# Kernel optimization log

Hardware: AMD Instinct MI355X
Metric: run time of the kernel (lower is better)

## Reference

```python
import jax, jax.numpy as jnp
import numpy as np

DIM = 512
NUM_HEADS = 8
HEAD_DIM = DIM // NUM_HEADS          # 64
KEY_DIM = int(HEAD_DIM * 0.5)        # 32
H_QKV = DIM + NUM_HEADS * KEY_DIM * 2  # 1024
SCALE = KEY_DIM ** -0.5
EPS = 1e-5


def bn(x, gamma, beta, mean, var):
    # inference-mode BatchNorm2d over channel axis 1 of NCHW
    inv = gamma / jnp.sqrt(var + EPS)
    return x * inv[None, :, None, None] + (beta - mean * inv)[None, :, None, None]


def conv1x1(x, w):
    # w: [out, in] (1x1 conv collapsed); x: NCHW
    return jnp.einsum('bchw,oc->bohw', x, w)


def dwconv3x3(x, w):
    # depthwise 3x3, 'same' padding; w: [C,1,3,3]
    return jax.lax.conv_general_dilated(
        x, w, window_strides=(1, 1), padding='SAME',
        feature_group_count=x.shape[1],
        dimension_numbers=('NCHW', 'OIHW', 'NCHW'))


def setup_inputs() -> dict:
    key = jax.random.key(0)
    ks = jax.random.split(key, 16)
    B, C, H, W = 8, DIM, 40, 40
    f = jax.random.normal
    inp = {
        'x': f(ks[0], (B, C, H, W), jnp.float32),
        'qkv_w': f(ks[1], (H_QKV, DIM), jnp.float32) * (1.0 / np.sqrt(DIM)),
        'qkv_gamma': 1.0 + 0.1 * f(ks[2], (H_QKV,), jnp.float32),
        'qkv_beta': 0.1 * f(ks[3], (H_QKV,), jnp.float32),
        'qkv_mean': 0.1 * f(ks[4], (H_QKV,), jnp.float32),
        'qkv_var': jax.random.uniform(ks[5], (H_QKV,), jnp.float32) + 0.5,
        'pe_w': f(ks[6], (DIM, 1, 3, 3), jnp.float32) * (1.0 / 3.0),
        'pe_gamma': 1.0 + 0.1 * f(ks[7], (DIM,), jnp.float32),
        'pe_beta': 0.1 * f(ks[8], (DIM,), jnp.float32),
        'pe_mean': 0.1 * f(ks[9], (DIM,), jnp.float32),
        'pe_var': jax.random.uniform(ks[10], (DIM,), jnp.float32) + 0.5,
        'proj_w': f(ks[11], (DIM, DIM), jnp.float32) * (1.0 / np.sqrt(DIM)),
        'proj_gamma': 1.0 + 0.1 * f(ks[12], (DIM,), jnp.float32),
        'proj_beta': 0.1 * f(ks[13], (DIM,), jnp.float32),
        'proj_mean': 0.1 * f(ks[14], (DIM,), jnp.float32),
        'proj_var': jax.random.uniform(ks[15], (DIM,), jnp.float32) + 0.5,
    }
    return inp


def reference(x, qkv_w, qkv_gamma, qkv_beta, qkv_mean, qkv_var,
              pe_w, pe_gamma, pe_beta, pe_mean, pe_var,
              proj_w, proj_gamma, proj_beta, proj_mean, proj_var):
    B, C, H, W = x.shape
    N = H * W
    qkv = bn(conv1x1(x, qkv_w), qkv_gamma, qkv_beta, qkv_mean, qkv_var)
    qkv = qkv.reshape(B, NUM_HEADS, KEY_DIM * 2 + HEAD_DIM, N)
    q = qkv[:, :, :KEY_DIM]                    # [B,h,kd,N]
    k = qkv[:, :, KEY_DIM:2 * KEY_DIM]         # [B,h,kd,N]
    v = qkv[:, :, 2 * KEY_DIM:]                # [B,h,hd,N]
    # attn = q^T @ k * scale -> [B,h,N,N], softmax over last dim
    attn = jnp.einsum('bhkn,bhkm->bhnm', q, k) * SCALE
    attn = jax.nn.softmax(attn, axis=-1)
    # out = v @ attn^T -> [B,h,hd,N]
    out = jnp.einsum('bhdm,bhnm->bhdn', v, attn).reshape(B, C, H, W)
    pe = bn(dwconv3x3(v.reshape(B, C, H, W), pe_w), pe_gamma, pe_beta, pe_mean, pe_var)
    y = out + pe
    y = bn(conv1x1(y, proj_w), proj_gamma, proj_beta, proj_mean, proj_var)
    return y
```

## Files before the change

### kernel.cpp

```cpp
#include <hip/hip_runtime.h>
#include <hip/hip_bf16.h>

#define EPS 1e-5f
#define SCALE 0.17677669529663687f
#define QSCALE 0.25500526817095634f

typedef __attribute__((ext_vector_type(8))) short bf16x8;
typedef __attribute__((ext_vector_type(4))) float f32x4;
typedef __attribute__((ext_vector_type(8))) unsigned short u16x8;

__device__ __forceinline__ unsigned short f2bf(float x) {
  union { float f; unsigned int u; } a; a.f = x;
  unsigned int r = a.u + 0x7FFFu + ((a.u >> 16) & 1u);
  return (unsigned short)(r >> 16);
}
__device__ __forceinline__ float bf2f(unsigned short u) {
  union { unsigned int u; float f; } a; a.u = ((unsigned int)u) << 16;
  return a.f;
}

__device__ __forceinline__ float fexp2(float x) {
#if __has_builtin(__builtin_amdgcn_exp2f)
  return __builtin_amdgcn_exp2f(x);
#else
  float r; asm("v_exp_f32 %0, %1" : "=v"(r) : "v"(x)); return r;
#endif
}

__device__ __forceinline__ void gload_lds16(const void* g, void* l) {
  __builtin_amdgcn_global_load_lds(
      (const __attribute__((address_space(1))) unsigned int*)g,
      (__attribute__((address_space(3))) unsigned int*)l, 16, 0, 0);
}

__device__ __forceinline__ unsigned int pack_bf_trunc(float a, float b) {
  return __builtin_amdgcn_perm(__float_as_uint(b), __float_as_uint(a), 0x07060302u);
}

__global__ __launch_bounds__(256) void cast_w_kernel(
    const float* __restrict__ qw, const float* __restrict__ pw,
    short* __restrict__ wq, short* __restrict__ wp) {
  int idx = blockIdx.x * 256 + threadIdx.x;
  const float4* src;
  ushort4* dst;
  if (idx < 131072) {
    src = (const float4*)qw + idx;
    dst = (ushort4*)wq + idx;
  } else {
    src = (const float4*)pw + (idx - 131072);
    dst = (ushort4*)wp + (idx - 131072);
  }
  float4 v = *src;
  ushort4 u;
  u.x = f2bf(v.x); u.y = f2bf(v.y); u.z = f2bf(v.z); u.w = f2bf(v.w);
  *dst = u;
}

__global__ __launch_bounds__(256) void transpose_cast_kernel(
    const float* __restrict__ X, short* __restrict__ XT) {
  __shared__ unsigned short T[64][72];
  const int b = blockIdx.z, c0 = blockIdx.x * 64, n0 = blockIdx.y * 64;
  const int t = threadIdx.x, nl = t & 63, w = t >> 6;
#pragma unroll
  for (int ci = 0; ci < 16; ++ci) {
    int cl = ci * 4 + w;
    T[nl][cl] = f2bf(X[((size_t)(b * 512 + c0 + cl)) * 1600 + n0 + nl]);
  }
  __syncthreads();
  const int n2 = t >> 2, cg = (t & 3) * 16;
  unsigned short* o = (unsigned short*)XT + ((size_t)(b * 1600 + n0 + n2)) * 512 + c0 + cg;
  *(u16x8*)&o[0] = *(const u16x8*)&T[n2][cg];
  *(u16x8*)&o[8] = *(const u16x8*)&T[n2][cg + 8];
}

__global__ __launch_bounds__(256) void transpose16_kernel(
    const short* __restrict__ S, short* __restrict__ D) {
  __shared__ unsigned short T[64][72];
  const int b = blockIdx.z, c0 = blockIdx.x * 64, n0 = blockIdx.y * 64;
  const int t = threadIdx.x, nl = t & 63, w = t >> 6;
  const unsigned short* Sp = (const unsigned short*)S;
#pragma unroll
  for (int ci = 0; ci < 16; ++ci) {
    int cl = ci * 4 + w;
    T[nl][cl] = Sp[((size_t)(b * 512 + c0 + cl)) * 1600 + n0 + nl];
  }
  __syncthreads();
  const int n2 = t >> 2, cg = (t & 3) * 16;
  unsigned short* o = (unsigned short*)D + ((size_t)(b * 1600 + n0 + n2)) * 512 + c0 + cg;
  *(u16x8*)&o[0] = *(const u16x8*)&T[n2][cg];
  *(u16x8*)&o[8] = *(const u16x8*)&T[n2][cg + 8];
}

__global__ __launch_bounds__(256) void qkv_mfma_kernel(
    const short* __restrict__ XT, const short* __restrict__ WQ,
    const float* __restrict__ gamma, const float* __restrict__ beta,
    const float* __restrict__ mean, const float* __restrict__ var,
    short* __restrict__ qT, short* __restrict__ kT,
    short* __restrict__ vb, short* __restrict__ vp) {
  __shared__ __align__(16) unsigned short As[128 * 32];
  __shared__ __align__(16) unsigned short Bs[128 * 32];

  const int t = threadIdx.x, w = t >> 6, lane = t & 63;
  const int quad = lane >> 4, l16 = lane & 15;
  const int wr = w >> 1, wc = w & 1;
  const int ngt = blockIdx.x, h = blockIdx.y;
  const int o0 = h * 128, ng0 = ngt * 128;

  const int srow = lane >> 2;
  const int sseg = (lane & 3) * 8;

  f32x4 acc[4][4];
#pragma unroll
  for (int mi = 0; mi < 4; ++mi)
#pragma unroll
    for (int nj = 0; nj < 4; ++nj) { acc[mi][nj][0]=0.f; acc[mi][nj][1]=0.f; acc[mi][nj][2]=0.f; acc[mi][nj][3]=0.f; }

  for (int kt = 0; kt < 16; ++kt) {
    const int c0 = kt * 32;
    if (kt) __syncthreads();
#pragma unroll
    for (int r = 0; r < 2; ++r) {
      const int row = (r * 4 + w) * 16 + srow;
      gload_lds16(WQ + (size_t)(o0 + row) * 512 + c0 + sseg, As + (r * 4 + w) * 512);
      gload_lds16(XT + (size_t)(ng0 + row) * 512 + c0 + sseg, Bs + (r * 4 + w) * 512);
    }
    __syncthreads();
    bf16x8 af[4], bfr[4];
#pragma unroll
    for (int i = 0; i < 4; ++i) {
      af[i]  = *(const bf16x8*)&As[(wr * 64 + i * 16 + l16) * 32 + quad * 8];
      bfr[i] = *(const bf16x8*)&Bs[(wc * 64 + i * 16 + l16) * 32 + quad * 8];
    }
#pragma unroll
    for (int mi = 0; mi < 4; ++mi)
#pragma unroll
      for (int nj = 0; nj < 4; ++nj)
        acc[mi][nj] = __builtin_amdgcn_mfma_f32_16x16x32_bf16(af[mi], bfr[nj], acc[mi][nj], 0, 0, 0);
  }

  const int ng_base = ng0 + wc * 64;
#pragma unroll
  for (int mi = 0; mi < 4; ++mi) {
    const int ol = wr * 64 + mi * 16 + quad * 4;
    const int ob = o0 + ol;
    float inv[4], add[4];
#pragma unroll
    for (int r = 0; r < 4; ++r) {
      inv[r] = gamma[ob + r] * rsqrtf(var[ob + r] + EPS);
      add[r] = beta[ob + r] - mean[ob + r] * inv[r];
    }
    const int region = wr * 2 + (mi >> 1);
    if (region == 0) {
      const int kk = mi * 16 + quad * 4;
#pragma unroll
      for (int nj = 0; nj < 4; ++nj) {
        int ng = ng_base + nj * 16 + l16;
        int b = ng / 1600, n = ng - b * 1600;
        ushort4 u;
        u.x = f2bf((acc[mi][nj][0] * inv[0] + add[0]) * QSCALE);
        u.y = f2bf((acc[mi][nj][1] * inv[1] + add[1]) * QSCALE);
        u.z = f2bf((acc[mi][nj][2] * inv[2] + add[2]) * QSCALE);
        u.w = f2bf((acc[mi][nj][3] * inv[3] + add[3]) * QSCALE);
        *(ushort4*)&qT[((size_t)(b * 8 + h) * 1600 + n) * 32 + kk] = u;
      }
    } else if (region == 1) {
      const int kk = (mi - 2) * 16 + quad * 4;
#pragma unroll
      for (int nj = 0; nj < 4; ++nj) {
        int ng = ng_base + nj * 16 + l16;
        int b = ng / 1600, n = ng - b * 1600;
        ushort4 u;
        u.x = f2bf(acc[mi][nj][0] * inv[0] + add[0]);
        u.y = f2bf(acc[mi][nj][1] * inv[1] + add[1]);
        u.z = f2bf(acc[mi][nj][2] * inv[2] + add[2]);
        u.w = f2bf(acc[mi][nj][3] * inv[3] + add[3]);
        *(ushort4*)&kT[((size_t)(b * 8 + h) * 1600 + n) * 32 + kk] = u;
      }
    } else {
      const int ch = h * 64 + (ol - 64);
      const int d0 = ol - 64;
#pragma unroll
      for (int nj = 0; nj < 4; ++nj) {
        int ng = ng_base + nj * 16 + l16;
        int b = ng / 1600, n = ng - b * 1600;
        unsigned short val[4];
#pragma unroll
        for (int r = 0; r < 4; ++r)
          val[r] = f2bf(acc[mi][nj][r] * inv[r] + add[r]);
#pragma unroll
        for (int r = 0; r < 4; ++r)
          ((unsigned short*)vb)[((size_t)(b * 512 + ch + r)) * 1600 + n] = val[r];
        unsigned short* dst = (unsigned short*)vp +
            ((size_t)(b * 8 + h) * 200 + (n >> 3)) * 512 + d0 * 8 + (n & 7);
#pragma unroll
        for (int r = 0; r < 4; ++r)
          dst[r * 8] = val[r];
      }
    }
  }
}

__global__ __launch_bounds__(256) void attn_mfma_kernel(
    const short* __restrict__ qT, const short* __restrict__ kT,
    const short* __restrict__ vp, short* __restrict__ ybf) {
  const int N = 1600;
  __shared__ __align__(16) unsigned short Vlds[2][8 * 512];
  const int t = threadIdx.x;
  const int w = t >> 6, lane = t & 63, quad = lane >> 4, l16 = lane & 15;
  const int bh = blockIdx.x, b = bh >> 3, h = bh & 7;
  int n0w = blockIdx.y * 128 + w * 32;
  if (n0w > 1568) n0w = 1568;

  const unsigned short* qTb = (const unsigned short*)qT + (size_t)bh * N * 32;
  const unsigned short* kTb = (const unsigned short*)kT + (size_t)bh * N * 32;
  const unsigned short* vpb = (const unsigned short*)vp + (size_t)bh * 102400;

  const bf16x8 qf0 = *(const bf16x8*)(qTb + (size_t)(n0w + l16) * 32 + quad * 8);
  const bf16x8 qf1 = *(const bf16x8*)(qTb + (size_t)(n0w + 16 + l16) * 32 + quad * 8);

  f32x4 acc0[4], acc1[4];
#pragma unroll
  for (int i = 0; i < 4; ++i) {
    acc0[i][0]=0.f; acc0[i][1]=0.f; acc0[i][2]=0.f; acc0[i][3]=0.f;
    acc1[i][0]=0.f; acc1[i][1]=0.f; acc1[i][2]=0.f; acc1[i][3]=0.f;
  }
  float den0 = 0.f, den1 = 0.f;
  const f32x4 zero4 = {0.f, 0.f, 0.f, 0.f};

  const int kperm = ((l16 & 12) << 1) + (l16 & 3);
  const unsigned short* kp = kTb + (size_t)kperm * 32 + quad * 8;

#define STAGE_V(BUF, IT) \
  { \
    _Pragma("unroll") \
    for (int j_ = 0; j_ < 2; ++j_) { \
      const int c_ = w * 2 + j_; \
      const int s_ = c_ >> 2, i_ = c_ & 3; \
      gload_lds16(vpb + (size_t)((IT) * 8 + s_ * 4 + quad) * 512 + (i_ * 16 + l16) * 8, \
                  &Vlds[BUF][c_ * 512]); \
    } \
  }

#define SUBTILE(K0, K1, V0, V1, V2, V3) \
  { \
    f32x4 s0_ = __builtin_amdgcn_mfma_f32_16x16x32_bf16(K0, qf0, zero4, 0, 0, 0); \
    f32x4 s1_ = __builtin_amdgcn_mfma_f32_16x16x32_bf16(K1, qf0, zero4, 0, 0, 0); \
    f32x4 t0_ = __builtin_amdgcn_mfma_f32_16x16x32_bf16(K0, qf1, zero4, 0, 0, 0); \
    f32x4 t1_ = __builtin_amdgcn_mfma_f32_16x16x32_bf16(K1, qf1, zero4, 0, 0, 0); \
    float a0_ = fexp2(s0_[0]), a1_ = fexp2(s0_[1]), a2_ = fexp2(s0_[2]), a3_ = fexp2(s0_[3]); \
    float a4_ = fexp2(s1_[0]), a5_ = fexp2(s1_[1]), a6_ = fexp2(s1_[2]), a7_ = fexp2(s1_[3]); \
    float b0_ = fexp2(t0_[0]), b1_ = fexp2(t0_[1]), b2_ = fexp2(t0_[2]), b3_ = fexp2(t0_[3]); \
    float b4_ = fexp2(t1_[0]), b5_ = fexp2(t1_[1]), b6_ = fexp2(t1_[2]), b7_ = fexp2(t1_[3]); \
    den0 += ((a0_ + a1_) + (a2_ + a3_)) + ((a4_ + a5_) + (a6_ + a7_)); \
    den1 += ((b0_ + b1_) + (b2_ + b3_)) + ((b4_ + b5_) + (b6_ + b7_)); \
    union { bf16x8 v; uint4 u; } pk0_, pk1_; \
    pk0_.u.x = pack_bf_trunc(a0_, a1_); pk0_.u.y = pack_bf_trunc(a2_, a3_); \
    pk0_.u.z = pack_bf_trunc(a4_, a5_); pk0_.u.w = pack_bf_trunc(a6_, a7_); \
    pk1_.u.x = pack_bf_trunc(b0_, b1_); pk1_.u.y = pack_bf_trunc(b2_, b3_); \
    pk1_.u.z = pack_bf_trunc(b4_, b5_); pk1_.u.w = pack_bf_trunc(b6_, b7_); \
    acc0[0] = __builtin_amdgcn_mfma_f32_16x16x32_bf16(pk0_.v, V0, acc0[0], 0, 0, 0); \
    acc1[0] = __builtin_amdgcn_mfma_f32_16x16x32_bf16(pk1_.v, V0, acc1[0], 0, 0, 0); \
    acc0[1] = __builtin_amdgcn_mfma_f32_16x16x32_bf16(pk0_.v, V1, acc0[1], 0, 0, 0); \
    acc1[1] = __builtin_amdgcn_mfma_f32_16x16x32_bf16(pk1_.v, V1, acc1[1], 0, 0, 0); \
    acc0[2] = __builtin_amdgcn_mfma_f32_16x16x32_bf16(pk0_.v, V2, acc0[2], 0, 0, 0); \
    acc1[2] = __builtin_amdgcn_mfma_f32_16x16x32_bf16(pk1_.v, V2, acc1[2], 0, 0, 0); \
    acc0[3] = __builtin_amdgcn_mfma_f32_16x16x32_bf16(pk0_.v, V3, acc0[3], 0, 0, 0); \
    acc1[3] = __builtin_amdgcn_mfma_f32_16x16x32_bf16(pk1_.v, V3, acc1[3], 0, 0, 0); \
  }

  STAGE_V(0, 0);

#pragma unroll 1
  for (int it = 0; it < 25; ++it) {
    const int cur = it & 1;
    __syncthreads();
    if (it + 1 < 25) STAGE_V(cur ^ 1, it + 1);

    const unsigned short* kpm = kp + (size_t)it * 2048;
    const bf16x8 ka0 = *(const bf16x8*)(kpm);
    const bf16x8 ka1 = *(const bf16x8*)(kpm + 128);
    const bf16x8 kb0 = *(const bf16x8*)(kpm + 1024);
    const bf16x8 kb1 = *(const bf16x8*)(kpm + 1152);
    const unsigned short* Lc = &Vlds[cur][lane * 8];
    const bf16x8 va0 = *(const bf16x8*)(Lc);
    const bf16x8 va1 = *(const bf16x8*)(Lc + 512);
    const bf16x8 va2 = *(const bf16x8*)(Lc + 1024);
    const bf16x8 va3 = *(const bf16x8*)(Lc + 1536);
    const bf16x8 vb0_ = *(const bf16x8*)(Lc + 2048);
    const bf16x8 vb1_ = *(const bf16x8*)(Lc + 2560);
    const bf16x8 vb2_ = *(const bf16x8*)(Lc + 3072);
    const bf16x8 vb3_ = *(const bf16x8*)(Lc + 3584);

    SUBTILE(ka0, ka1, va0, va1, va2, va3);
    SUBTILE(kb0, kb1, vb0_, vb1_, vb2_, vb3_);
  }
#undef SUBTILE
#undef STAGE_V

  den0 += __shfl_xor(den0, 16, 64);
  den0 += __shfl_xor(den0, 32, 64);
  den1 += __shfl_xor(den1, 16, 64);
  den1 += __shfl_xor(den1, 32, 64);
  const float rden0 = 1.f / den0;
  const float rden1 = 1.f / den1;
  float dv0[4], dv1[4];
#pragma unroll
  for (int r = 0; r < 4; ++r) {
    dv0[r] = __shfl(rden0, quad * 4 + r, 64);
    dv1[r] = __shfl(rden1, quad * 4 + r, 64);
  }

  unsigned short* yb = (unsigned short*)ybf + ((size_t)b * 512 + h * 64) * N;
#pragma unroll
  for (int i = 0; i < 4; ++i) {
    const size_t rowo = (size_t)(i * 16 + l16) * N;
    ushort4 o4;
    o4.x = f2bf(acc0[i][0] * dv0[0]);
    o4.y = f2bf(acc0[i][1] * dv0[1]);
    o4.z = f2bf(acc0[i][2] * dv0[2]);
    o4.w = f2bf(acc0[i][3] * dv0[3]);
    *(ushort4*)&yb[rowo + n0w + quad * 4] = o4;
    o4.x = f2bf(acc1[i][0] * dv1[0]);
    o4.y = f2bf(acc1[i][1] * dv1[1]);
    o4.z = f2bf(acc1[i][2] * dv1[2]);
    o4.w = f2bf(acc1[i][3] * dv1[3]);
    *(ushort4*)&yb[rowo + n0w + 16 + quad * 4] = o4;
  }
}

__global__ __launch_bounds__(256) void pe_kernel(
    const short* __restrict__ Ybf, const short* __restrict__ VB,
    const float* __restrict__ pw,
    const float* __restrict__ gamma, const float* __restrict__ beta,
    const float* __restrict__ mean, const float* __restrict__ var,
    short* __restrict__ YB) {
  __shared__ __align__(16) unsigned short V[4 * 42 * 56];
  __shared__ float wlds[36];
  __shared__ float invs[4], adds[4];

  const int t = threadIdx.x;
  const int b = blockIdx.y, c0 = blockIdx.x * 4;

  const u16x8 z = {0, 0, 0, 0, 0, 0, 0, 0};
  for (int k = t; k < 1176; k += 256)
    *(u16x8*)&V[k * 8] = z;
  if (t < 36) wlds[t] = pw[c0 * 9 + t];
  if (t < 4) {
    int c = c0 + t;
    float inv = gamma[c] * rsqrtf(var[c] + EPS);
    invs[t] = inv;
    adds[t] = beta[c] - mean[c] * inv;
  }
  __syncthreads();

  for (int u = t; u < 800; u += 256) {
    int ch = u / 200, j = u - ch * 200;
    int row = j / 5, col8 = (j - row * 5) * 8;
    u16x8 d = *(const u16x8*)((const unsigned short*)VB +
        ((size_t)(b * 512 + c0 + ch) * 1600 + row * 40 + col8));
    *(u16x8*)&V[ch * 2352 + (row + 1) * 56 + 8 + col8] = d;
  }
  __syncthreads();

#pragma unroll 1
  for (int k = 0; k < 25; ++k) {
    int o = k * 256 + t;
    int ch = o / 1600, n = o - ch * 1600;
    int hh = n / 40, ww = n - hh * 40;
    const unsigned short* Vc = &V[ch * 2352 + (hh + 1) * 56 + 8 + ww];
    const float* wk = &wlds[ch * 9];
    float s = 0.f;
#pragma unroll
    for (int dy = 0; dy < 3; ++dy)
#pragma unroll
      for (int dx = 0; dx < 3; ++dx)
        s += wk[dy * 3 + dx] * bf2f(Vc[(dy - 1) * 56 + (dx - 1)]);
    size_t idx = (size_t)(b * 512 + c0 + ch) * 1600 + n;
    float val = bf2f(((const unsigned short*)Ybf)[idx]) + s * invs[ch] + adds[ch];
    YB[idx] = (short)f2bf(val);
  }
}

__global__ __launch_bounds__(256) void proj_mfma_kernel(
    const short* __restrict__ YT, const short* __restrict__ WP,
    const float* __restrict__ gamma, const float* __restrict__ beta,
    const float* __restrict__ mean, const float* __restrict__ var,
    float* __restrict__ OUT) {
  __shared__ __align__(16) unsigned short As[64 * 32];
  __shared__ __align__(16) unsigned short Bs[128 * 32];

  const int t = threadIdx.x, w = t >> 6, lane = t & 63;
  const int quad = lane >> 4, l16 = lane & 15;
  const int wr = w >> 1, wc = w & 1;
  const int ngt = blockIdx.x;
  const int o0 = blockIdx.y * 64;
  const int ng0 = ngt * 128;

  const int srow = lane >> 2;
  const int sseg = (lane & 3) * 8;

  f32x4 acc[2][4];
#pragma unroll
  for (int mi = 0; mi < 2; ++mi)
#pragma unroll
    for (int nj = 0; nj < 4; ++nj) { acc[mi][nj][0]=0.f; acc[mi][nj][1]=0.f; acc[mi][nj][2]=0.f; acc[mi][nj][3]=0.f; }

  for (int kt = 0; kt < 16; ++kt) {
    const int c0 = kt * 32;
    if (kt) __syncthreads();
    {
      const int row = w * 16 + srow;
      gload_lds16(WP + (size_t)(o0 + row) * 512 + c0 + sseg, As + w * 512);
    }
#pragma unroll
    for (int r = 0; r < 2; ++r) {
      const int row = (r * 4 + w) * 16 + srow;
      gload_lds16(YT + (size_t)(ng0 + row) * 512 + c0 + sseg, Bs + (r * 4 + w) * 512);
    }
    __syncthreads();
    bf16x8 af[2], bfr[4];
#pragma unroll
    for (int i = 0; i < 2; ++i)
      af[i] = *(const bf16x8*)&As[(wr * 32 + i * 16 + l16) * 32 + quad * 8];
#pragma unroll
    for (int i = 0; i < 4; ++i)
      bfr[i] = *(const bf16x8*)&Bs[(wc * 64 + i * 16 + l16) * 32 + quad * 8];
#pragma unroll
    for (int mi = 0; mi < 2; ++mi)
#pragma unroll
      for (int nj = 0; nj < 4; ++nj)
        acc[mi][nj] = __builtin_amdgcn_mfma_f32_16x16x32_bf16(af[mi], bfr[nj], acc[mi][nj], 0, 0, 0);
  }

  const int ng_base = ng0 + wc * 64;
#pragma unroll
  for (int mi = 0; mi < 2; ++mi) {
    const int ob = o0 + wr * 32 + mi * 16 + quad * 4;
    float inv[4], add[4];
#pragma unroll
    for (int r = 0; r < 4; ++r) {
      inv[r] = gamma[ob + r] * rsqrtf(var[ob + r] + EPS);
      add[r] = beta[ob + r] - mean[ob + r] * inv[r];
    }
#pragma unroll
    for (int nj = 0; nj < 4; ++nj) {
      int ng = ng_base + nj * 16 + l16;
      int b = ng / 1600, n = ng - b * 1600;
#pragma unroll
      for (int r = 0; r < 4; ++r)
        OUT[((size_t)(b * 512 + ob + r)) * 1600 + n] = acc[mi][nj][r] * inv[r] + add[r];
    }
  }
}

extern "C" void kernel_launch(void* const* d_in, const int* in_sizes, int n_in,
                              void* d_out, int out_size, void* d_ws, size_t ws_size,
                              hipStream_t stream) {
  const float* x          = (const float*)d_in[0];
  const float* qkv_w      = (const float*)d_in[1];
  const float* qkv_gamma  = (const float*)d_in[2];
  const float* qkv_beta   = (const float*)d_in[3];
  const float* qkv_mean   = (const float*)d_in[4];
  const float* qkv_var    = (const float*)d_in[5];
  const float* pe_w       = (const float*)d_in[6];
  const float* pe_gamma   = (const float*)d_in[7];
  const float* pe_beta    = (const float*)d_in[8];
  const float* pe_mean    = (const float*)d_in[9];
  const float* pe_var     = (const float*)d_in[10];
  const float* proj_w     = (const float*)d_in[11];
  const float* proj_gamma = (const float*)d_in[12];
  const float* proj_beta  = (const float*)d_in[13];
  const float* proj_mean  = (const float*)d_in[14];
  const float* proj_var   = (const float*)d_in[15];
  float* out = (float*)d_out;

  float* ws_a = (float*)d_ws;
  short* ybf_attn = (short*)d_ws;
  short* vp   = ybf_attn + (size_t)6553600;
  short* qT   = (short*)(ws_a + (size_t)6553600);
  short* kT   = qT + (size_t)3276800;
  short* vb   = kT + (size_t)3276800;
  short* xT   = vb + (size_t)6553600;
  short* wq   = xT + (size_t)6553600;
  short* wp   = wq + (size_t)524288;
  short* yT   = xT;
  short* ybf_pe = qT;

  cast_w_kernel<<<768, 256, 0, stream>>>(qkv_w, proj_w, wq, wp);
  {
    dim3 grid(8, 25, 8), block(256);
    transpose_cast_kernel<<<grid, block, 0, stream>>>(x, xT);
  }
  {
    dim3 grid(100, 8), block(256);
    qkv_mfma_kernel<<<grid, block, 0, stream>>>(
        xT, wq, qkv_gamma, qkv_beta, qkv_mean, qkv_var, qT, kT, vb, vp);
  }
  {
    dim3 grid(64, 13), block(256);
    attn_mfma_kernel<<<grid, block, 0, stream>>>(qT, kT, vp, ybf_attn);
  }
  {
    dim3 grid(128, 8), block(256);
    pe_kernel<<<grid, block, 0, stream>>>(
        ybf_attn, vb, pe_w, pe_gamma, pe_beta, pe_mean, pe_var, ybf_pe);
  }
  {
    dim3 grid(8, 25, 8), block(256);
    transpose16_kernel<<<grid, block, 0, stream>>>(ybf_pe, yT);
  }
  {
    dim3 grid(100, 8), block(256);
    proj_mfma_kernel<<<grid, block, 0, stream>>>(
        yT, wp, proj_gamma, proj_beta, proj_mean, proj_var, out);
  }
}
```

Baseline: 238.4 us.

## Split attention key range across wave pairs and reduce partial results via LDS

Each block now handles 64 queries instead of 128. Its four waves form two query tiles, and each tile is split across two waves, each covering half of the keys. V and K fragments are loaded straight from global memory into registers with software double-buffering, replacing the LDS-staged V and the per-iteration __syncthreads. Partial accumulators and softmax denominators are combined through LDS at the end. The grid grows to 64x25 blocks, which removes the clamped overlapping tail tile and raises parallelism. The cost is more redundant global K/V traffic and an extra LDS reduction step.

```diff
diff --git a/kernel.cpp b/kernel.cpp
--- a/kernel.cpp
+++ b/kernel.cpp
@@ -204,12 +204,13 @@
     const short* __restrict__ qT, const short* __restrict__ kT,
     const short* __restrict__ vp, short* __restrict__ ybf) {
   const int N = 1600;
-  __shared__ __align__(16) unsigned short Vlds[2][8 * 512];
+  __shared__ __align__(16) float accL[4][2][2][64][4];
+  __shared__ float denL[4][2][16];
   const int t = threadIdx.x;
   const int w = t >> 6, lane = t & 63, quad = lane >> 4, l16 = lane & 15;
+  const int qt = w >> 1, kh = w & 1;
   const int bh = blockIdx.x, b = bh >> 3, h = bh & 7;
-  int n0w = blockIdx.y * 128 + w * 32;
-  if (n0w > 1568) n0w = 1568;
+  const int n0w = blockIdx.y * 64 + qt * 32;
 
   const unsigned short* qTb = (const unsigned short*)qT + (size_t)bh * N * 32;
   const unsigned short* kTb = (const unsigned short*)kT + (size_t)bh * N * 32;
@@ -228,20 +229,22 @@
   const f32x4 zero4 = {0.f, 0.f, 0.f, 0.f};
 
   const int kperm = ((l16 & 12) << 1) + (l16 & 3);
-  const unsigned short* kp = kTb + (size_t)kperm * 32 + quad * 8;
-
-#define STAGE_V(BUF, IT) \
+  const unsigned short* kp = kTb + (size_t)(kh * 800 + kperm) * 32 + quad * 8;
+  const unsigned short* vq = vpb + (size_t)(kh * 100 + quad) * 512 + l16 * 8;
+
+#define LOADT(MT, K0, K1, V0, V1, V2, V3) \
   { \
-    _Pragma("unroll") \
-    for (int j_ = 0; j_ < 2; ++j_) { \
-      const int c_ = w * 2 + j_; \
-      const int s_ = c_ >> 2, i_ = c_ & 3; \
-      gload_lds16(vpb + (size_t)((IT) * 8 + s_ * 4 + quad) * 512 + (i_ * 16 + l16) * 8, \
-                  &Vlds[BUF][c_ * 512]); \
-    } \
-  }
-
-#define SUBTILE(K0, K1, V0, V1, V2, V3) \
+    const unsigned short* kpm_ = kp + (size_t)(MT) * 1024; \
+    const unsigned short* vqm_ = vq + (size_t)(MT) * 2048; \
+    K0 = *(const bf16x8*)kpm_; \
+    K1 = *(const bf16x8*)(kpm_ + 128); \
+    V0 = *(const bf16x8*)(vqm_); \
+    V1 = *(const bf16x8*)(vqm_ + 128); \
+    V2 = *(const bf16x8*)(vqm_ + 256); \
+    V3 = *(const bf16x8*)(vqm_ + 384); \
+  }
+
+#define COMP(K0, K1, V0, V1, V2, V3) \
   { \
     f32x4 s0_ = __builtin_amdgcn_mfma_f32_16x16x32_bf16(K0, qf0, zero4, 0, 0, 0); \
     f32x4 s1_ = __builtin_amdgcn_mfma_f32_16x16x32_bf16(K1, qf0, zero4, 0, 0, 0); \
@@ -268,62 +271,59 @@
     acc1[3] = __builtin_amdgcn_mfma_f32_16x16x32_bf16(pk1_.v, V3, acc1[3], 0, 0, 0); \
   }
 
-  STAGE_V(0, 0);
+  bf16x8 ck0, ck1, cv0, cv1, cv2, cv3, nk0, nk1, nv0, nv1, nv2, nv3;
+  LOADT(0, ck0, ck1, cv0, cv1, cv2, cv3);
 
 #pragma unroll 1
-  for (int it = 0; it < 25; ++it) {
-    const int cur = it & 1;
-    __syncthreads();
-    if (it + 1 < 25) STAGE_V(cur ^ 1, it + 1);
-
-    const unsigned short* kpm = kp + (size_t)it * 2048;
-    const bf16x8 ka0 = *(const bf16x8*)(kpm);
-    const bf16x8 ka1 = *(const bf16x8*)(kpm + 128);
-    const bf16x8 kb0 = *(const bf16x8*)(kpm + 1024);
-    const bf16x8 kb1 = *(const bf16x8*)(kpm + 1152);
-    const unsigned short* Lc = &Vlds[cur][lane * 8];
-    const bf16x8 va0 = *(const bf16x8*)(Lc);
-    const bf16x8 va1 = *(const bf16x8*)(Lc + 512);
-    const bf16x8 va2 = *(const bf16x8*)(Lc + 1024);
-    const bf16x8 va3 = *(const bf16x8*)(Lc + 1536);
-    const bf16x8 vb0_ = *(const bf16x8*)(Lc + 2048);
-    const bf16x8 vb1_ = *(const bf16x8*)(Lc + 2560);
-    const bf16x8 vb2_ = *(const bf16x8*)(Lc + 3072);
-    const bf16x8 vb3_ = *(const bf16x8*)(Lc + 3584);
-
-    SUBTILE(ka0, ka1, va0, va1, va2, va3);
-    SUBTILE(kb0, kb1, vb0_, vb1_, vb2_, vb3_);
-  }
-#undef SUBTILE
-#undef STAGE_V
+  for (int mt2 = 0; mt2 < 12; ++mt2) {
+    LOADT(2 * mt2 + 1, nk0, nk1, nv0, nv1, nv2, nv3);
+    COMP(ck0, ck1, cv0, cv1, cv2, cv3);
+    LOADT(2 * mt2 + 2, ck0, ck1, cv0, cv1, cv2, cv3);
+    COMP(nk0, nk1, nv0, nv1, nv2, nv3);
+  }
+  COMP(ck0, ck1, cv0, cv1, cv2, cv3);
+#undef COMP
+#undef LOADT
 
   den0 += __shfl_xor(den0, 16, 64);
   den0 += __shfl_xor(den0, 32, 64);
   den1 += __shfl_xor(den1, 16, 64);
   den1 += __shfl_xor(den1, 32, 64);
-  const float rden0 = 1.f / den0;
-  const float rden1 = 1.f / den1;
+
+#pragma unroll
+  for (int ii = 0; ii < 2; ++ii) {
+    const int i = (1 - kh) * 2 + ii;
+    *(f32x4*)&accL[w][0][ii][lane][0] = acc0[i];
+    *(f32x4*)&accL[w][1][ii][lane][0] = acc1[i];
+  }
+  if (quad == 0) { denL[w][0][l16] = den0; denL[w][1][l16] = den1; }
+  __syncthreads();
+
+  const int pw = w ^ 1;
   float dv0[4], dv1[4];
 #pragma unroll
   for (int r = 0; r < 4; ++r) {
-    dv0[r] = __shfl(rden0, quad * 4 + r, 64);
-    dv1[r] = __shfl(rden1, quad * 4 + r, 64);
+    dv0[r] = 1.f / (denL[w][0][quad * 4 + r] + denL[pw][0][quad * 4 + r]);
+    dv1[r] = 1.f / (denL[w][1][quad * 4 + r] + denL[pw][1][quad * 4 + r]);
   }
 
   unsigned short* yb = (unsigned short*)ybf + ((size_t)b * 512 + h * 64) * N;
 #pragma unroll
-  for (int i = 0; i < 4; ++i) {
+  for (int ii = 0; ii < 2; ++ii) {
+    const int i = kh * 2 + ii;
+    f32x4 a0 = acc0[i] + *(const f32x4*)&accL[pw][0][ii][lane][0];
+    f32x4 a1 = acc1[i] + *(const f32x4*)&accL[pw][1][ii][lane][0];
     const size_t rowo = (size_t)(i * 16 + l16) * N;
     ushort4 o4;
-    o4.x = f2bf(acc0[i][0] * dv0[0]);
-    o4.y = f2bf(acc0[i][1] * dv0[1]);
-    o4.z = f2bf(acc0[i][2] * dv0[2]);
-    o4.w = f2bf(acc0[i][3] * dv0[3]);
+    o4.x = f2bf(a0[0] * dv0[0]);
+    o4.y = f2bf(a0[1] * dv0[1]);
+    o4.z = f2bf(a0[2] * dv0[2]);
+    o4.w = f2bf(a0[3] * dv0[3]);
     *(ushort4*)&yb[rowo + n0w + quad * 4] = o4;
-    o4.x = f2bf(acc1[i][0] * dv1[0]);
-    o4.y = f2bf(acc1[i][1] * dv1[1]);
-    o4.z = f2bf(acc1[i][2] * dv1[2]);
-    o4.w = f2bf(acc1[i][3] * dv1[3]);
+    o4.x = f2bf(a1[0] * dv1[0]);
+    o4.y = f2bf(a1[1] * dv1[1]);
+    o4.z = f2bf(a1[2] * dv1[2]);
+    o4.w = f2bf(a1[3] * dv1[3]);
     *(ushort4*)&yb[rowo + n0w + 16 + quad * 4] = o4;
   }
 }
@@ -497,7 +497,7 @@
         xT, wq, qkv_gamma, qkv_beta, qkv_mean, qkv_var, qT, kT, vb, vp);
   }
   {
-    dim3 grid(64, 13), block(256);
+    dim3 grid(64, 25), block(256);
     attn_mfma_kernel<<<grid, block, 0, stream>>>(qT, kT, vp, ybf_attn);
   }
   {
```

Measured after the change: 237.1 us. Within noise of the previous version (-0.5%).

## Replace LDS-staged V tiles with triple-buffered register prefetch from global

Applied to the files above, without the earlier changes.

The attention kernel no longer stages V tiles through double-buffered shared memory behind a per-iteration __syncthreads. Each wave now loads its K and V fragments straight from global memory into registers, using a three-deep software pipeline over 32-key tiles. Waves whose query rows fall past the end now return early instead of recomputing a clamped tile, which is safe because no barrier remains. This removes block-wide synchronisation and LDS traffic. In exchange, every wave in a block fetches the same V data separately through the caches, and the extra prefetch buffers raise register pressure.

```diff
diff --git a/kernel.cpp b/kernel.cpp
--- a/kernel.cpp
+++ b/kernel.cpp
@@ -204,12 +204,11 @@
     const short* __restrict__ qT, const short* __restrict__ kT,
     const short* __restrict__ vp, short* __restrict__ ybf) {
   const int N = 1600;
-  __shared__ __align__(16) unsigned short Vlds[2][8 * 512];
   const int t = threadIdx.x;
   const int w = t >> 6, lane = t & 63, quad = lane >> 4, l16 = lane & 15;
   const int bh = blockIdx.x, b = bh >> 3, h = bh & 7;
-  int n0w = blockIdx.y * 128 + w * 32;
-  if (n0w > 1568) n0w = 1568;
+  const int n0w = blockIdx.y * 128 + w * 32;
+  if (n0w >= 1600) return;
 
   const unsigned short* qTb = (const unsigned short*)qT + (size_t)bh * N * 32;
   const unsigned short* kTb = (const unsigned short*)kT + (size_t)bh * N * 32;
@@ -229,19 +228,21 @@
 
   const int kperm = ((l16 & 12) << 1) + (l16 & 3);
   const unsigned short* kp = kTb + (size_t)kperm * 32 + quad * 8;
-
-#define STAGE_V(BUF, IT) \
+  const unsigned short* vq = vpb + (size_t)quad * 512 + l16 * 8;
+
+#define LOADT(MT, K0, K1, V0, V1, V2, V3) \
   { \
-    _Pragma("unroll") \
-    for (int j_ = 0; j_ < 2; ++j_) { \
-      const int c_ = w * 2 + j_; \
-      const int s_ = c_ >> 2, i_ = c_ & 3; \
-      gload_lds16(vpb + (size_t)((IT) * 8 + s_ * 4 + quad) * 512 + (i_ * 16 + l16) * 8, \
-                  &Vlds[BUF][c_ * 512]); \
-    } \
-  }
-
-#define SUBTILE(K0, K1, V0, V1, V2, V3) \
+    const unsigned short* kpm_ = kp + (size_t)(MT) * 1024; \
+    const unsigned short* vqm_ = vq + (size_t)(MT) * 2048; \
+    K0 = *(const bf16x8*)kpm_; \
+    K1 = *(const bf16x8*)(kpm_ + 128); \
+    V0 = *(const bf16x8*)(vqm_); \
+    V1 = *(const bf16x8*)(vqm_ + 128); \
+    V2 = *(const bf16x8*)(vqm_ + 256); \
+    V3 = *(const bf16x8*)(vqm_ + 384); \
+  }
+
+#define COMP(K0, K1, V0, V1, V2, V3) \
   { \
     f32x4 s0_ = __builtin_amdgcn_mfma_f32_16x16x32_bf16(K0, qf0, zero4, 0, 0, 0); \
     f32x4 s1_ = __builtin_amdgcn_mfma_f32_16x16x32_bf16(K1, qf0, zero4, 0, 0, 0); \
@@ -268,34 +269,26 @@
     acc1[3] = __builtin_amdgcn_mfma_f32_16x16x32_bf16(pk1_.v, V3, acc1[3], 0, 0, 0); \
   }
 
-  STAGE_V(0, 0);
+  bf16x8 ak0, ak1, av0, av1, av2, av3;
+  bf16x8 bk0, bk1, bv0, bv1, bv2, bv3;
+  bf16x8 ck0, ck1, cv0, cv1, cv2, cv3;
+  LOADT(0, ak0, ak1, av0, av1, av2, av3);
+  LOADT(1, bk0, bk1, bv0, bv1, bv2, bv3);
 
 #pragma unroll 1
-  for (int it = 0; it < 25; ++it) {
-    const int cur = it & 1;
-    __syncthreads();
-    if (it + 1 < 25) STAGE_V(cur ^ 1, it + 1);
-
-    const unsigned short* kpm = kp + (size_t)it * 2048;
-    const bf16x8 ka0 = *(const bf16x8*)(kpm);
-    const bf16x8 ka1 = *(const bf16x8*)(kpm + 128);
-    const bf16x8 kb0 = *(const bf16x8*)(kpm + 1024);
-    const bf16x8 kb1 = *(const bf16x8*)(kpm + 1152);
-    const unsigned short* Lc = &Vlds[cur][lane * 8];
-    const bf16x8 va0 = *(const bf16x8*)(Lc);
-    const bf16x8 va1 = *(const bf16x8*)(Lc + 512);
-    const bf16x8 va2 = *(const bf16x8*)(Lc + 1024);
-    const bf16x8 va3 = *(const bf16x8*)(Lc + 1536);
-    const bf16x8 vb0_ = *(const bf16x8*)(Lc + 2048);
-    const bf16x8 vb1_ = *(const bf16x8*)(Lc + 2560);
-    const bf16x8 vb2_ = *(const bf16x8*)(Lc + 3072);
-    const bf16x8 vb3_ = *(const bf16x8*)(Lc + 3584);
-
-    SUBTILE(ka0, ka1, va0, va1, va2, va3);
-    SUBTILE(kb0, kb1, vb0_, vb1_, vb2_, vb3_);
-  }
-#undef SUBTILE
-#undef STAGE_V
+  for (int it = 0; it < 16; ++it) {
+    const int mt = it * 3;
+    LOADT(mt + 2, ck0, ck1, cv0, cv1, cv2, cv3);
+    COMP(ak0, ak1, av0, av1, av2, av3);
+    LOADT(mt + 3, ak0, ak1, av0, av1, av2, av3);
+    COMP(bk0, bk1, bv0, bv1, bv2, bv3);
+    LOADT(mt + 4, bk0, bk1, bv0, bv1, bv2, bv3);
+    COMP(ck0, ck1, cv0, cv1, cv2, cv3);
+  }
+  COMP(ak0, ak1, av0, av1, av2, av3);
+  COMP(bk0, bk1, bv0, bv1, bv2, bv3);
+#undef COMP
+#undef LOADT
 
   den0 += __shfl_xor(den0, 16, 64);
   den0 += __shfl_xor(den0, 32, 64);
```

New measurement: 237.2 us. No clear change (-0.5%).
